# Kernel tuning notes

Measured on AMD Instinct MI355X. Metric: run time of the kernel, lower is better.

The kernel has to match this reference:

```python
import jax, jax.numpy as jnp
import numpy as np

E = 512   # embed_dim
H = 8     # num_heads
D = E // H  # head_dim


def setup_inputs() -> dict:
    key = jax.random.key(0)
    ks = jax.random.split(key, 13)
    B, Nq, Nk = 4, 2048, 2048
    query = jax.random.normal(ks[0], (B, Nq, E), dtype=jnp.float32)
    key_t = jax.random.normal(ks[1], (B, Nk, E), dtype=jnp.float32)
    value = jax.random.normal(ks[2], (B, Nk, E), dtype=jnp.float32)
    geometry_mask = jax.random.bernoulli(ks[3], 0.5, (B, Nq, Nk))  # True = keep
    s = 1.0 / np.sqrt(E)
    Wq = jax.random.normal(ks[4], (E, E), dtype=jnp.float32) * s
    bq = jax.random.normal(ks[5], (E,), dtype=jnp.float32) * 0.01
    Wk = jax.random.normal(ks[6], (E, E), dtype=jnp.float32) * s
    bk = jax.random.normal(ks[7], (E,), dtype=jnp.float32) * 0.01
    Wv = jax.random.normal(ks[8], (E, E), dtype=jnp.float32) * s
    bv = jax.random.normal(ks[9], (E,), dtype=jnp.float32) * 0.01
    Wo = jax.random.normal(ks[10], (E, E), dtype=jnp.float32) * s
    bo = jax.random.normal(ks[11], (E,), dtype=jnp.float32) * 0.01
    return {"query": query, "key": key_t, "value": value,
            "geometry_mask": geometry_mask,
            "Wq": Wq, "bq": bq, "Wk": Wk, "bk": bk,
            "Wv": Wv, "bv": bv, "Wo": Wo, "bo": bo}


def reference(query, key, value, geometry_mask, Wq, bq, Wk, bk, Wv, bv, Wo, bo):
    B, Nq, _ = query.shape
    Nk = key.shape[1]
    scale = D ** -0.5
    # projections -> (B, H, N, D)
    Q = (query @ Wq + bq).reshape(B, Nq, H, D).transpose(0, 2, 1, 3)
    K = (key @ Wk + bk).reshape(B, Nk, H, D).transpose(0, 2, 1, 3)
    V = (value @ Wv + bv).reshape(B, Nk, H, D).transpose(0, 2, 1, 3)
    scores = jnp.einsum('bhqd,bhkd->bhqk', Q, K) * scale
    mask = geometry_mask[:, None, :, :]  # (B,1,Nq,Nk), True = keep
    scores = jnp.where(mask, scores, -jnp.inf)
    attn = jax.nn.softmax(scores, axis=-1)  # dropout p=0 (eval)
    out = jnp.einsum('bhqk,bhkd->bhqd', attn, V)
    out = out.transpose(0, 2, 1, 3).reshape(B, Nq, E)
    return out @ Wo + bo
```

## Files before the change

### kernel.cpp

```cpp
#include <hip/hip_runtime.h>
#include <stdint.h>


typedef __attribute__((ext_vector_type(8))) short bf16x8;
typedef __attribute__((ext_vector_type(4))) float f32x4;

#define SCLQ 0.18033688011112042f

static __device__ __forceinline__ unsigned short f2bf(float f) {
    union { float f; unsigned u; } x; x.f = f;
    unsigned r = x.u + 0x7fffu + ((x.u >> 16) & 1u);
    return (unsigned short)(r >> 16);
}

static __device__ __forceinline__ f32x4 mfma16(bf16x8 a, bf16x8 b, f32x4 c) {
    return __builtin_amdgcn_mfma_f32_16x16x32_bf16(a, b, c, 0, 0, 0);
}

#define GLOAD_LDS16(g, l)                                                            \
    __builtin_amdgcn_global_load_lds((const __attribute__((address_space(1))) void*)(g), \
                                     (__attribute__((address_space(3))) void*)(l), 16, 0, 0)


__global__ __launch_bounds__(256) void cvt_x_kernel(
    const float* __restrict__ xq, const float* __restrict__ xk, const float* __restrict__ xv,
    short* __restrict__ oq, short* __restrict__ ok, short* __restrict__ ov)
{
    const float* src = (blockIdx.y == 0) ? xq : (blockIdx.y == 1) ? xk : xv;
    short* dst = (blockIdx.y == 0) ? oq : (blockIdx.y == 1) ? ok : ov;
    size_t i = (size_t)blockIdx.x * 256 + threadIdx.x;
    float4 v = ((const float4*)src)[i];
    short4 o;
    o.x = (short)f2bf(v.x); o.y = (short)f2bf(v.y);
    o.z = (short)f2bf(v.z); o.w = (short)f2bf(v.w);
    ((short4*)dst)[i] = o;
}

__global__ __launch_bounds__(256) void cvt_wt_kernel(
    const float* __restrict__ Wq, const float* __restrict__ Wk,
    const float* __restrict__ Wv, const float* __restrict__ Wo,
    short* __restrict__ WqT, short* __restrict__ WkT,
    short* __restrict__ WvT, short* __restrict__ WoT)
{
    int z = blockIdx.y;
    const float* W = (z == 0) ? Wq : (z == 1) ? Wk : (z == 2) ? Wv : Wo;
    short* WT = (z == 0) ? WqT : (z == 1) ? WkT : (z == 2) ? WvT : WoT;
    int t = blockIdx.x * 256 + threadIdx.x;
    int n = t & 511;
    int k0 = (t >> 9) * 8;
    union { short s[8]; int4 v; } u;
#pragma unroll
    for (int j = 0; j < 8; ++j) u.s[j] = (short)f2bf(W[(size_t)(k0 + j) * 512 + n]);
    *(int4*)(WT + (size_t)n * 512 + k0) = u.v;
}

__global__ __launch_bounds__(256) void pack_mask_kernel(
    const int* __restrict__ mask, unsigned long long* __restrict__ mp)
{
    int lane = threadIdx.x & 63;
    int row = blockIdx.x * 4 + (threadIdx.x >> 6);
    const int* mrow = mask + (size_t)row * 2048;
#pragma unroll 4
    for (int w = 0; w < 32; ++w) {
        unsigned long long bits = __ballot(mrow[w * 64 + lane] != 0);
        if (lane == 0) mp[(size_t)row * 32 + w] = bits;
    }
}

static __device__ __forceinline__ void gemm_body(
    const short* __restrict__ A, const short* __restrict__ BT,
    const float* __restrict__ bias, void* __restrict__ Cout, int mode,
    char* lds, int bx, int by)
{
    const int tid = threadIdx.x;
    const int lane = tid & 63;
    const int wid = tid >> 6;
    const int l15 = lane & 15, l4 = lane >> 4;
    const int m0 = by * 128;
    const int n0 = bx * 128;
    const int wr = wid >> 1, wc = wid & 1;

    f32x4 zero = {0.f, 0.f, 0.f, 0.f};
    f32x4 acc[4][4];
#pragma unroll
    for (int i = 0; i < 4; ++i)
#pragma unroll
        for (int j = 0; j < 4; ++j) acc[i][j] = zero;

    char* Alds = lds;
    char* Blds = lds + 16384;

    for (int t = 0; t < 8; ++t) {
        const int k0 = t * 64;
#pragma unroll
        for (int s = 0; s < 4; ++s) {
            int p = s * 256 + tid;
            int r = p >> 3, c = p & 7;
            GLOAD_LDS16(A + (size_t)(m0 + r) * 512 + k0 + 8 * (c ^ (r & 7)),
                        Alds + s * 4096 + wid * 1024);
            GLOAD_LDS16(BT + (size_t)(n0 + r) * 512 + k0 + 8 * (c ^ (r & 7)),
                        Blds + s * 4096 + wid * 1024);
        }
        __syncthreads();
#pragma unroll
        for (int ks = 0; ks < 2; ++ks) {
            bf16x8 af[4], bfr[4];
#pragma unroll
            for (int mb = 0; mb < 4; ++mb) {
                int row = wr * 64 + mb * 16 + l15;
                af[mb] = *(const bf16x8*)(Alds + row * 128 +
                                          ((ks * 64 + l4 * 16) ^ ((row & 7) << 4)));
            }
#pragma unroll
            for (int nb = 0; nb < 4; ++nb) {
                int row = wc * 64 + nb * 16 + l15;
                bfr[nb] = *(const bf16x8*)(Blds + row * 128 +
                                           ((ks * 64 + l4 * 16) ^ ((row & 7) << 4)));
            }
#pragma unroll
            for (int mb = 0; mb < 4; ++mb)
#pragma unroll
                for (int nb = 0; nb < 4; ++nb)
                    acc[mb][nb] = mfma16(af[mb], bfr[nb], acc[mb][nb]);
        }
        __syncthreads();
    }

#pragma unroll
    for (int nb = 0; nb < 4; ++nb) {
        int n = n0 + wc * 64 + nb * 16 + l15;
        float bv = bias[n];
#pragma unroll
        for (int mb = 0; mb < 4; ++mb) {
#pragma unroll
            for (int r = 0; r < 4; ++r) {
                int m = m0 + wr * 64 + mb * 16 + l4 * 4 + r;
                float val = acc[mb][nb][r] + bv;
                if (mode == 0) val *= SCLQ;
                if (mode == 3) {
                    ((float*)Cout)[(size_t)m * 512 + n] = val;
                } else {
                    int b = m >> 11, tok = m & 2047;
                    int h = n >> 6, d = n & 63;
                    short* o = (short*)Cout;
                    if (mode == 2)
                        o[((size_t)(b * 8 + h) * 64 + d) * 2048 + tok] = (short)f2bf(val);
                    else
                        o[((size_t)(b * 8 + h) * 2048 + tok) * 64 + d] = (short)f2bf(val);
                }
            }
        }
    }
}

__global__ __launch_bounds__(256) void gemm_qkv_kernel(
    const short* __restrict__ Xq, const short* __restrict__ Xk, const short* __restrict__ Xv,
    const short* __restrict__ WqT, const short* __restrict__ WkT, const short* __restrict__ WvT,
    const float* __restrict__ bq, const float* __restrict__ bk, const float* __restrict__ bv,
    short* __restrict__ Qw, short* __restrict__ Kw, short* __restrict__ VTw)
{
    __shared__ char lds[32768];
    int z = blockIdx.z;
    const short* A = (z == 0) ? Xq : (z == 1) ? Xk : Xv;
    const short* BT = (z == 0) ? WqT : (z == 1) ? WkT : WvT;
    const float* bias = (z == 0) ? bq : (z == 1) ? bk : bv;
    void* Cout = (z == 0) ? (void*)Qw : (z == 1) ? (void*)Kw : (void*)VTw;
    gemm_body(A, BT, bias, Cout, z, lds, blockIdx.x, blockIdx.y);
}

__global__ __launch_bounds__(256) void gemm_kernel(
    const short* __restrict__ A, const short* __restrict__ BT,
    const float* __restrict__ bias, void* __restrict__ Cout, int mode)
{
    __shared__ char lds[32768];
    gemm_body(A, BT, bias, Cout, mode, lds, blockIdx.x, blockIdx.y);
}

__global__ __launch_bounds__(512) void attn_kernel(
    const short* __restrict__ Q, const short* __restrict__ K,
    const short* __restrict__ VT, const unsigned long long* __restrict__ mp,
    short* __restrict__ AO)
{
    __shared__ char lds[32768];
    const int tid = threadIdx.x;
    const int lane = tid & 63;
    const int wid = tid >> 6;
    const int l15 = lane & 15, l4 = lane >> 4;
    const int lid = blockIdx.x;
    const int xcd = lid & 7, jj = lid >> 3;
    const int bhi = (xcd << 2) | (jj >> 4);
    const int b = bhi >> 3, h = bhi & 7;
    const int q0 = (jj & 15) * 128 + wid * 16;
    const short* Qp = Q + ((size_t)bhi * 2048 + q0) * 64;
    const short* Kp = K + (size_t)bhi * 2048 * 64;
    const short* Vp = VT + (size_t)bhi * 64 * 2048;

    const int srow = tid >> 3;
    const int sgo = 8 * ((tid & 7) ^ (srow & 7));
    const int swl = l15 & 7;

    bf16x8 qb[2];
#pragma unroll
    for (int dc = 0; dc < 2; ++dc)
        qb[dc] = *(const bf16x8*)(Qp + l15 * 64 + dc * 32 + l4 * 8);

    const f32x4 zero = {0.f, 0.f, 0.f, 0.f};
    f32x4 o[4];
#pragma unroll
    for (int dt = 0; dt < 4; ++dt) o[dt] = zero;
    float mrun = -1e30f, lrun = 0.f;

    const unsigned long long* mr0 = mp + ((size_t)b * 2048 + q0 + l15) * 32;

    GLOAD_LDS16(Kp + (size_t)srow * 64 + sgo, lds + wid * 1024);
    GLOAD_LDS16(Vp + (size_t)srow * 2048 + sgo, lds + 16384 + wid * 1024);
    unsigned long long mw0 = mr0[0];
    __syncthreads();

    for (int kt = 0; kt < 32; ++kt) {
        const int cur = kt & 1;
        char* Kc = lds + cur * 8192;
        char* Vc = lds + 16384 + cur * 8192;
        if (kt < 31) {
            GLOAD_LDS16(Kp + ((size_t)(kt + 1) * 64 + srow) * 64 + sgo,
                        lds + (cur ^ 1) * 8192 + wid * 1024);
            GLOAD_LDS16(Vp + (size_t)srow * 2048 + (kt + 1) * 64 + sgo,
                        lds + 16384 + (cur ^ 1) * 8192 + wid * 1024);
        }
        unsigned long long mn0 = (kt < 31) ? mr0[kt + 1] : 0ull;

        bf16x8 ka[4][2];
#pragma unroll
        for (int tb = 0; tb < 4; ++tb)
#pragma unroll
            for (int dc = 0; dc < 2; ++dc)
                ka[tb][dc] = *(const bf16x8*)(Kc + (tb * 16 + l15) * 128 +
                                              16 * ((dc * 4 + l4) ^ swl));

        f32x4 sv[4];
#pragma unroll
        for (int tb = 0; tb < 4; ++tb) {
            unsigned u0 = (unsigned)(mw0 >> (tb * 16 + l4 * 4));
            f32x4 i0;
#pragma unroll
            for (int r = 0; r < 4; ++r)
                i0[r] = (u0 & (1u << r)) ? 0.f : -1e30f;
            sv[tb] = mfma16(ka[tb][1], qb[1], mfma16(ka[tb][0], qb[0], i0));
        }

        bf16x8 vb[4][2];
#pragma unroll
        for (int dt = 0; dt < 4; ++dt)
#pragma unroll
            for (int kb = 0; kb < 2; ++kb) {
                const char* vr = Vc + (dt * 16 + l15) * 128;
                uint2 x = *(const uint2*)(vr + 16 * ((kb * 4 + (l4 >> 1)) ^ swl) +
                                          (l4 & 1) * 8);
                uint2 y = *(const uint2*)(vr + 16 * ((kb * 4 + 2 + (l4 >> 1)) ^ swl) +
                                          (l4 & 1) * 8);
                uint4 t; t.x = x.x; t.y = x.y; t.z = y.x; t.w = y.y;
                vb[dt][kb] = *(bf16x8*)&t;
            }

        f32x4 m0v;
#pragma unroll
        for (int r = 0; r < 4; ++r)
            m0v[r] = fmaxf(fmaxf(sv[0][r], sv[1][r]), fmaxf(sv[2][r], sv[3][r]));
        float pm0 = fmaxf(fmaxf(m0v[0], m0v[1]), fmaxf(m0v[2], m0v[3]));
        pm0 = fmaxf(pm0, __shfl_xor(pm0, 16, 64));
        pm0 = fmaxf(pm0, __shfl_xor(pm0, 32, 64));

        if (__any(pm0 > mrun + 8.f)) {
            float mnew = fmaxf(mrun, pm0);
            float al = exp2f(mrun - mnew);
            mrun = mnew; lrun *= al;
#pragma unroll
            for (int r = 0; r < 4; ++r) {
                float alr = __shfl(al, l4 * 4 + r, 64);
#pragma unroll
                for (int dt = 0; dt < 4; ++dt) o[dt][r] *= alr;
            }
        }

#pragma unroll
        for (int tb = 0; tb < 4; ++tb)
#pragma unroll
            for (int r = 0; r < 4; ++r)
                sv[tb][r] = exp2f(sv[tb][r] - mrun);
        {
            f32x4 t0 = (sv[0] + sv[1]) + (sv[2] + sv[3]);
            lrun += (t0[0] + t0[1]) + (t0[2] + t0[3]);
        }

        bf16x8 pa[2];
#define PACK8(DST, SA, SB)                                                              \
        { uint4 t_;                                                                     \
          asm("v_cvt_pk_bf16_f32 %0, %1, %2" : "=v"(t_.x) : "v"(SA[0]), "v"(SA[1]));    \
          asm("v_cvt_pk_bf16_f32 %0, %1, %2" : "=v"(t_.y) : "v"(SA[2]), "v"(SA[3]));    \
          asm("v_cvt_pk_bf16_f32 %0, %1, %2" : "=v"(t_.z) : "v"(SB[0]), "v"(SB[1]));    \
          asm("v_cvt_pk_bf16_f32 %0, %1, %2" : "=v"(t_.w) : "v"(SB[2]), "v"(SB[3]));    \
          DST = *(bf16x8*)&t_; }
        PACK8(pa[0], sv[0], sv[1])
        PACK8(pa[1], sv[2], sv[3])
#undef PACK8

#pragma unroll
        for (int dt = 0; dt < 4; ++dt)
            o[dt] = mfma16(pa[1], vb[dt][1], mfma16(pa[0], vb[dt][0], o[dt]));

        mw0 = mn0;
        __syncthreads();
    }

    {
        float lt = lrun;
        lt += __shfl_xor(lt, 16, 64);
        lt += __shfl_xor(lt, 32, 64);
        float inv = 1.0f / lt;
#pragma unroll
        for (int r = 0; r < 4; ++r) {
            float invr = __shfl(inv, l4 * 4 + r, 64);
            size_t base = ((size_t)b * 2048 + q0 + l4 * 4 + r) * 512 + h * 64;
#pragma unroll
            for (int dt = 0; dt < 4; ++dt)
                AO[base + dt * 16 + l15] = (short)f2bf(o[dt][r] * invr);
        }
    }
}

extern "C" void kernel_launch(void* const* d_in, const int* in_sizes, int n_in,
                              void* d_out, int out_size, void* d_ws, size_t ws_size,
                              hipStream_t stream) {
    const float* q  = (const float*)d_in[0];
    const float* k  = (const float*)d_in[1];
    const float* v  = (const float*)d_in[2];
    const int*   gm = (const int*)d_in[3];
    const float* Wq = (const float*)d_in[4];  const float* bq = (const float*)d_in[5];
    const float* Wk = (const float*)d_in[6];  const float* bk = (const float*)d_in[7];
    const float* Wv = (const float*)d_in[8];  const float* bv = (const float*)d_in[9];
    const float* Wo = (const float*)d_in[10]; const float* bo = (const float*)d_in[11];

    char* ws = (char*)d_ws;
    short* Xq  = (short*)(ws + 0);
    short* Xk  = (short*)(ws + 8388608);
    short* Xv  = (short*)(ws + 16777216);
    short* WqT = (short*)(ws + 25165824);
    short* WkT = (short*)(ws + 25690112);
    short* WvT = (short*)(ws + 26214400);
    short* WoT = (short*)(ws + 26738688);
    short* Qw  = (short*)(ws + 27262976);
    short* Kw  = (short*)(ws + 35651584);
    short* VTw = (short*)(ws + 44040192);
    short* AO  = (short*)(ws + 52428800);
    unsigned long long* MP = (unsigned long long*)(ws + 60817408);

    cvt_x_kernel<<<dim3(4096, 3), 256, 0, stream>>>(q, k, v, Xq, Xk, Xv);
    cvt_wt_kernel<<<dim3(128, 4), 256, 0, stream>>>(Wq, Wk, Wv, Wo, WqT, WkT, WvT, WoT);
    pack_mask_kernel<<<dim3(2048), 256, 0, stream>>>(gm, MP);

    gemm_qkv_kernel<<<dim3(4, 64, 3), 256, 0, stream>>>(Xq, Xk, Xv, WqT, WkT, WvT,
                                                        bq, bk, bv, Qw, Kw, VTw);

    attn_kernel<<<dim3(512), 512, 0, stream>>>(Qw, Kw, VTw, MP, AO);

    gemm_kernel<<<dim3(4, 64), 256, 0, stream>>>(AO, WoT, bo, (void*)d_out, 3);
}
```

Baseline: 168.3 us.

## Double key tile to 128 per barrier and fold running max into mask bias

The attention loop now stages 128 keys per iteration: four global-to-LDS loads per thread into a 64 KB double buffer, processed as two 64-key halves. This halves the number of __syncthreads barriers and per-iteration prefetch overheads. It also folds the running-max subtraction into the MFMA accumulator init by using -mrun as the unmasked bias, which removes a subtract before each exp2, and it moves the max shuffles inside the rare rescale branch. Doubling LDS per block may reduce occupancy.

```diff
diff --git a/kernel.cpp b/kernel.cpp
--- a/kernel.cpp
+++ b/kernel.cpp
@@ -181,7 +181,7 @@
     const short* __restrict__ VT, const unsigned long long* __restrict__ mp,
     short* __restrict__ AO)
 {
-    __shared__ char lds[32768];
+    __shared__ char lds[65536];
     const int tid = threadIdx.x;
     const int lane = tid & 63;
     const int wid = tid >> 6;
@@ -195,122 +195,132 @@
     const short* Kp = K + (size_t)bhi * 2048 * 64;
     const short* Vp = VT + (size_t)bhi * 64 * 2048;
 
-    const int srow = tid >> 3;
-    const int sgo = 8 * ((tid & 7) ^ (srow & 7));
+    const int krow = tid >> 3;
+    const int kgo  = 8 * ((tid & 7) ^ (krow & 7));
+    const int vrow0 = tid >> 4;
+    const int vgo   = 8 * ((tid & 15) ^ (vrow0 & 7));
+    const int vrow1 = 32 + vrow0;
     const int swl = l15 & 7;
+
+#define STAGE(KT, BUF)                                                               \
+    {                                                                                \
+        const short* Kn = Kp + (size_t)(KT) * 128 * 64;                              \
+        char* Kd = lds + (BUF) * 16384;                                              \
+        GLOAD_LDS16(Kn + (size_t)krow * 64 + kgo, Kd + wid * 1024);                  \
+        GLOAD_LDS16(Kn + (size_t)(64 + krow) * 64 + kgo, Kd + 8192 + wid * 1024);    \
+        const short* Vn = Vp + (KT) * 128;                                           \
+        char* Vd = lds + 32768 + (BUF) * 16384;                                      \
+        GLOAD_LDS16(Vn + (size_t)vrow0 * 2048 + vgo, Vd + wid * 1024);               \
+        GLOAD_LDS16(Vn + (size_t)vrow1 * 2048 + vgo, Vd + 8192 + wid * 1024);        \
+    }
 
     bf16x8 qb[2];
 #pragma unroll
     for (int dc = 0; dc < 2; ++dc)
         qb[dc] = *(const bf16x8*)(Qp + l15 * 64 + dc * 32 + l4 * 8);
 
-    const f32x4 zero = {0.f, 0.f, 0.f, 0.f};
     f32x4 o[4];
 #pragma unroll
-    for (int dt = 0; dt < 4; ++dt) o[dt] = zero;
-    float mrun = -1e30f, lrun = 0.f;
+    for (int dt = 0; dt < 4; ++dt) o[dt] = f32x4{0.f, 0.f, 0.f, 0.f};
+    float mrun = 0.f, lrun = 0.f;
 
     const unsigned long long* mr0 = mp + ((size_t)b * 2048 + q0 + l15) * 32;
 
-    GLOAD_LDS16(Kp + (size_t)srow * 64 + sgo, lds + wid * 1024);
-    GLOAD_LDS16(Vp + (size_t)srow * 2048 + sgo, lds + 16384 + wid * 1024);
-    unsigned long long mw0 = mr0[0];
+    STAGE(0, 0)
+    ulonglong2 mwv = *(const ulonglong2*)(mr0);
     __syncthreads();
 
-    for (int kt = 0; kt < 32; ++kt) {
+#define HALF(H, MW)                                                                  \
+    {                                                                                \
+        bf16x8 ka[4][2];                                                             \
+        _Pragma("unroll") for (int tb = 0; tb < 4; ++tb)                             \
+            _Pragma("unroll") for (int dc = 0; dc < 2; ++dc)                         \
+                ka[tb][dc] = *(const bf16x8*)(Kc + (H) * 8192 +                      \
+                                              (tb * 16 + l15) * 128 +                \
+                                              16 * ((dc * 4 + l4) ^ swl));           \
+        bf16x8 vb[4][2];                                                             \
+        _Pragma("unroll") for (int dt = 0; dt < 4; ++dt)                             \
+            _Pragma("unroll") for (int kb = 0; kb < 2; ++kb) {                       \
+                const char* vr = Vc + (dt * 16 + l15) * 256;                         \
+                uint2 x = *(const uint2*)(vr +                                       \
+                    16 * (((H) * 8 + kb * 4 + (l4 >> 1)) ^ swl) + (l4 & 1) * 8);     \
+                uint2 y = *(const uint2*)(vr +                                       \
+                    16 * (((H) * 8 + kb * 4 + 2 + (l4 >> 1)) ^ swl) + (l4 & 1) * 8); \
+                uint4 t; t.x = x.x; t.y = x.y; t.z = y.x; t.w = y.y;                 \
+                vb[dt][kb] = *(bf16x8*)&t;                                           \
+            }                                                                        \
+        const float nm = -mrun;                                                      \
+        unsigned long long u64 = (MW) >> (l4 * 4);                                   \
+        unsigned ulo = (unsigned)u64, uhi = (unsigned)(u64 >> 32);                   \
+        f32x4 sv[4];                                                                 \
+        _Pragma("unroll") for (int tb = 0; tb < 4; ++tb) {                           \
+            unsigned us = (tb & 2) ? uhi : ulo;                                      \
+            f32x4 i0;                                                                \
+            _Pragma("unroll") for (int r = 0; r < 4; ++r)                            \
+                i0[r] = (us & (1u << (((tb & 1) << 4) + r))) ? nm : -1e30f;          \
+            sv[tb] = mfma16(ka[tb][1], qb[1], mfma16(ka[tb][0], qb[0], i0));         \
+        }                                                                            \
+        float pml;                                                                   \
+        {                                                                            \
+            f32x4 m0v;                                                               \
+            _Pragma("unroll") for (int r = 0; r < 4; ++r)                            \
+                m0v[r] = fmaxf(fmaxf(sv[0][r], sv[1][r]), fmaxf(sv[2][r], sv[3][r]));\
+            pml = fmaxf(fmaxf(m0v[0], m0v[1]), fmaxf(m0v[2], m0v[3]));               \
+        }                                                                            \
+        if (__any(pml > 8.f)) {                                                      \
+            float pm = fmaxf(pml, __shfl_xor(pml, 16, 64));                          \
+            pm = fmaxf(pm, __shfl_xor(pm, 32, 64));                                  \
+            float dm = fmaxf(pm, 0.f);                                               \
+            float al = exp2f(-dm);                                                   \
+            mrun += dm;                                                              \
+            lrun *= al;                                                              \
+            _Pragma("unroll") for (int r = 0; r < 4; ++r) {                          \
+                float alr = __shfl(al, l4 * 4 + r, 64);                              \
+                _Pragma("unroll") for (int dt = 0; dt < 4; ++dt) o[dt][r] *= alr;    \
+            }                                                                        \
+            _Pragma("unroll") for (int tb = 0; tb < 4; ++tb)                         \
+                _Pragma("unroll") for (int r = 0; r < 4; ++r) sv[tb][r] -= dm;       \
+        }                                                                            \
+        _Pragma("unroll") for (int tb = 0; tb < 4; ++tb)                             \
+            _Pragma("unroll") for (int r = 0; r < 4; ++r)                            \
+                sv[tb][r] = exp2f(sv[tb][r]);                                        \
+        {                                                                            \
+            f32x4 t0 = (sv[0] + sv[1]) + (sv[2] + sv[3]);                            \
+            lrun += (t0[0] + t0[1]) + (t0[2] + t0[3]);                               \
+        }                                                                            \
+        bf16x8 pa[2];                                                                \
+        {                                                                            \
+            uint4 t_;                                                                \
+            asm("v_cvt_pk_bf16_f32 %0, %1, %2" : "=v"(t_.x) : "v"(sv[0][0]), "v"(sv[0][1])); \
+            asm("v_cvt_pk_bf16_f32 %0, %1, %2" : "=v"(t_.y) : "v"(sv[0][2]), "v"(sv[0][3])); \
+            asm("v_cvt_pk_bf16_f32 %0, %1, %2" : "=v"(t_.z) : "v"(sv[1][0]), "v"(sv[1][1])); \
+            asm("v_cvt_pk_bf16_f32 %0, %1, %2" : "=v"(t_.w) : "v"(sv[1][2]), "v"(sv[1][3])); \
+            pa[0] = *(bf16x8*)&t_;                                                   \
+            asm("v_cvt_pk_bf16_f32 %0, %1, %2" : "=v"(t_.x) : "v"(sv[2][0]), "v"(sv[2][1])); \
+            asm("v_cvt_pk_bf16_f32 %0, %1, %2" : "=v"(t_.y) : "v"(sv[2][2]), "v"(sv[2][3])); \
+            asm("v_cvt_pk_bf16_f32 %0, %1, %2" : "=v"(t_.z) : "v"(sv[3][0]), "v"(sv[3][1])); \
+            asm("v_cvt_pk_bf16_f32 %0, %1, %2" : "=v"(t_.w) : "v"(sv[3][2]), "v"(sv[3][3])); \
+            pa[1] = *(bf16x8*)&t_;                                                   \
+        }                                                                            \
+        _Pragma("unroll") for (int dt = 0; dt < 4; ++dt)                             \
+            o[dt] = mfma16(pa[1], vb[dt][1], mfma16(pa[0], vb[dt][0], o[dt]));       \
+    }
+
+    for (int kt = 0; kt < 16; ++kt) {
         const int cur = kt & 1;
-        char* Kc = lds + cur * 8192;
-        char* Vc = lds + 16384 + cur * 8192;
-        if (kt < 31) {
-            GLOAD_LDS16(Kp + ((size_t)(kt + 1) * 64 + srow) * 64 + sgo,
-                        lds + (cur ^ 1) * 8192 + wid * 1024);
-            GLOAD_LDS16(Vp + (size_t)srow * 2048 + (kt + 1) * 64 + sgo,
-                        lds + 16384 + (cur ^ 1) * 8192 + wid * 1024);
-        }
-        unsigned long long mn0 = (kt < 31) ? mr0[kt + 1] : 0ull;
-
-        bf16x8 ka[4][2];
-#pragma unroll
-        for (int tb = 0; tb < 4; ++tb)
-#pragma unroll
-            for (int dc = 0; dc < 2; ++dc)
-                ka[tb][dc] = *(const bf16x8*)(Kc + (tb * 16 + l15) * 128 +
-                                              16 * ((dc * 4 + l4) ^ swl));
-
-        f32x4 sv[4];
-#pragma unroll
-        for (int tb = 0; tb < 4; ++tb) {
-            unsigned u0 = (unsigned)(mw0 >> (tb * 16 + l4 * 4));
-            f32x4 i0;
-#pragma unroll
-            for (int r = 0; r < 4; ++r)
-                i0[r] = (u0 & (1u << r)) ? 0.f : -1e30f;
-            sv[tb] = mfma16(ka[tb][1], qb[1], mfma16(ka[tb][0], qb[0], i0));
-        }
-
-        bf16x8 vb[4][2];
-#pragma unroll
-        for (int dt = 0; dt < 4; ++dt)
-#pragma unroll
-            for (int kb = 0; kb < 2; ++kb) {
-                const char* vr = Vc + (dt * 16 + l15) * 128;
-                uint2 x = *(const uint2*)(vr + 16 * ((kb * 4 + (l4 >> 1)) ^ swl) +
-                                          (l4 & 1) * 8);
-                uint2 y = *(const uint2*)(vr + 16 * ((kb * 4 + 2 + (l4 >> 1)) ^ swl) +
-                                          (l4 & 1) * 8);
-                uint4 t; t.x = x.x; t.y = x.y; t.z = y.x; t.w = y.y;
-                vb[dt][kb] = *(bf16x8*)&t;
-            }
-
-        f32x4 m0v;
-#pragma unroll
-        for (int r = 0; r < 4; ++r)
-            m0v[r] = fmaxf(fmaxf(sv[0][r], sv[1][r]), fmaxf(sv[2][r], sv[3][r]));
-        float pm0 = fmaxf(fmaxf(m0v[0], m0v[1]), fmaxf(m0v[2], m0v[3]));
-        pm0 = fmaxf(pm0, __shfl_xor(pm0, 16, 64));
-        pm0 = fmaxf(pm0, __shfl_xor(pm0, 32, 64));
-
-        if (__any(pm0 > mrun + 8.f)) {
-            float mnew = fmaxf(mrun, pm0);
-            float al = exp2f(mrun - mnew);
-            mrun = mnew; lrun *= al;
-#pragma unroll
-            for (int r = 0; r < 4; ++r) {
-                float alr = __shfl(al, l4 * 4 + r, 64);
-#pragma unroll
-                for (int dt = 0; dt < 4; ++dt) o[dt][r] *= alr;
-            }
-        }
-
-#pragma unroll
-        for (int tb = 0; tb < 4; ++tb)
-#pragma unroll
-            for (int r = 0; r < 4; ++r)
-                sv[tb][r] = exp2f(sv[tb][r] - mrun);
-        {
-            f32x4 t0 = (sv[0] + sv[1]) + (sv[2] + sv[3]);
-            lrun += (t0[0] + t0[1]) + (t0[2] + t0[3]);
-        }
-
-        bf16x8 pa[2];
-#define PACK8(DST, SA, SB)                                                              \
-        { uint4 t_;                                                                     \
-          asm("v_cvt_pk_bf16_f32 %0, %1, %2" : "=v"(t_.x) : "v"(SA[0]), "v"(SA[1]));    \
-          asm("v_cvt_pk_bf16_f32 %0, %1, %2" : "=v"(t_.y) : "v"(SA[2]), "v"(SA[3]));    \
-          asm("v_cvt_pk_bf16_f32 %0, %1, %2" : "=v"(t_.z) : "v"(SB[0]), "v"(SB[1]));    \
-          asm("v_cvt_pk_bf16_f32 %0, %1, %2" : "=v"(t_.w) : "v"(SB[2]), "v"(SB[3]));    \
-          DST = *(bf16x8*)&t_; }
-        PACK8(pa[0], sv[0], sv[1])
-        PACK8(pa[1], sv[2], sv[3])
-#undef PACK8
-
-#pragma unroll
-        for (int dt = 0; dt < 4; ++dt)
-            o[dt] = mfma16(pa[1], vb[dt][1], mfma16(pa[0], vb[dt][0], o[dt]));
-
-        mw0 = mn0;
+        char* Kc = lds + cur * 16384;
+        char* Vc = lds + 32768 + cur * 16384;
+        if (kt < 15) STAGE(kt + 1, cur ^ 1)
+        ulonglong2 mwn;
+        mwn.x = 0; mwn.y = 0;
+        if (kt < 15) mwn = *(const ulonglong2*)(mr0 + 2 * kt + 2);
+        HALF(0, mwv.x)
+        HALF(1, mwv.y)
+        mwv = mwn;
         __syncthreads();
     }
+#undef HALF
+#undef STAGE
 
     {
         float lt = lrun;
```

After: 165.9 us. No clear change (-1.4%).
